# Performance work log

Measured on AMD Instinct MI355X. Metric: run time of the kernel, lower is better.

## Reference

```python
import jax, jax.numpy as jnp
import numpy as np

C = 128          # channels
N = 100000       # cells per rank (rank 0,1,2)
E_A0, E_A1, E_I1, E_I2 = 400000, 400000, 200000, 300000
NI = {"a0": 3, "a1": 6, "i1": 3, "i2": 6}   # invariant feature dims per relation
FACTOR = {"u0": 2, "u1": 3, "u2": 2}          # update-MLP concat factors


def setup_inputs() -> dict:
    key = jax.random.key(0)
    ks = iter(jax.random.split(key, 64))
    d = {}
    for name in ("f0", "f1", "f2"):
        d[name] = jax.random.normal(next(ks), (N, C), dtype=jnp.float32)
    for name, E in (("a0", E_A0), ("a1", E_A1), ("i1", E_I1), ("i2", E_I2)):
        d[name + "_send"] = jax.random.randint(next(ks), (E,), 0, N)
        d[name + "_recv"] = jax.random.randint(next(ks), (E,), 0, N)
        d["inv_" + name] = jax.random.uniform(next(ks), (E, NI[name]), dtype=jnp.float32)
        fin = 2 * C + NI[name]
        d[name + "_W1"] = jax.random.normal(next(ks), (fin, C), dtype=jnp.float32) / np.sqrt(fin)
        d[name + "_b1"] = jnp.zeros((C,), jnp.float32)
        d[name + "_W2"] = jax.random.normal(next(ks), (C, C), dtype=jnp.float32) / np.sqrt(C)
        d[name + "_b2"] = jnp.zeros((C,), jnp.float32)
        d[name + "_Wg"] = jax.random.normal(next(ks), (C, 1), dtype=jnp.float32) / np.sqrt(C)
        d[name + "_bg"] = jnp.zeros((1,), jnp.float32)
    for name, f in FACTOR.items():
        d[name + "_W1"] = jax.random.normal(next(ks), (f * C, C), dtype=jnp.float32) / np.sqrt(f * C)
        d[name + "_b1"] = jnp.zeros((C,), jnp.float32)
        d[name + "_W2"] = jax.random.normal(next(ks), (C, C), dtype=jnp.float32) / np.sqrt(C)
        d[name + "_b2"] = jnp.zeros((C,), jnp.float32)
    return d


def _econv(x_src, x_tgt, send, recv, inv, W1, b1, W2, b2, Wg, bg):
    # EConv: gather endpoints, per-edge 2-layer MLP on [x_s, x_t, invariants],
    # gated by a sigmoid edge-inference scalar (with_weighted_message=True).
    m = jnp.concatenate([x_src[send], x_tgt[recv], inv], axis=1)  # (E, 2C+ninv)
    m = jax.nn.silu(m @ W1 + b1)                                   # (E, C)
    m = jax.nn.silu(m @ W2 + b2)                                   # (E, C)
    gate = jax.nn.sigmoid(m @ Wg + bg)                             # (E, 1)
    return m * gate


def _aggregate(msg, recv, n):
    # ScatterAggregation: scatter-sum to target cells, then silu update.
    return jax.nn.silu(jax.ops.segment_sum(msg, recv, num_segments=n))


def _update(h, W1, b1, W2, b2):
    # update MLP: Linear -> SiLU -> Linear
    return jax.nn.silu(h @ W1 + b1) @ W2 + b2


def reference(f0, f1, f2,
              a0_send, a0_recv, inv_a0, a0_W1, a0_b1, a0_W2, a0_b2, a0_Wg, a0_bg,
              a1_send, a1_recv, inv_a1, a1_W1, a1_b1, a1_W2, a1_b2, a1_Wg, a1_bg,
              i1_send, i1_recv, inv_i1, i1_W1, i1_b1, i1_W2, i1_b2, i1_Wg, i1_bg,
              i2_send, i2_recv, inv_i2, i2_W1, i2_b1, i2_W2, i2_b2, i2_Wg, i2_bg,
              u0_W1, u0_b1, u0_W2, u0_b2,
              u1_W1, u1_b1, u1_W2, u1_b2,
              u2_W1, u2_b1, u2_W2, u2_b2):
    # same-rank messages (rank 0 and 1 adjacency)
    m_a0 = _aggregate(_econv(f0, f0, a0_send, a0_recv, inv_a0, a0_W1, a0_b1, a0_W2, a0_b2, a0_Wg, a0_bg), a0_recv, N)
    m_a1 = _aggregate(_econv(f1, f1, a1_send, a1_recv, inv_a1, a1_W1, a1_b1, a1_W2, a1_b2, a1_Wg, a1_bg), a1_recv, N)
    # low-to-high messages (incidence rank 0->1 and 1->2)
    m_i1 = _aggregate(_econv(f0, f1, i1_send, i1_recv, inv_i1, i1_W1, i1_b1, i1_W2, i1_b2, i1_Wg, i1_bg), i1_recv, N)
    m_i2 = _aggregate(_econv(f1, f2, i2_send, i2_recv, inv_i2, i2_W1, i2_b1, i2_W2, i2_b2, i2_Wg, i2_bg), i2_recv, N)
    # concat features with aggregated messages, update, residual add
    h0 = _update(jnp.concatenate([f0, m_a0], axis=1), u0_W1, u0_b1, u0_W2, u0_b2)
    h1 = _update(jnp.concatenate([f1, m_a1, m_i1], axis=1), u1_W1, u1_b1, u1_W2, u1_b2)
    h2 = _update(jnp.concatenate([f2, m_i2], axis=1), u2_W1, u2_b1, u2_W2, u2_b2)
    return jnp.stack([f0 + h0, f1 + h1, f2 + h2])  # (3, N, C)
```

## Files before the change

### kernel.cpp

```cpp
#include <hip/hip_runtime.h>
#include <hip/hip_bf16.h>
#include <cstdint>
#include <cstddef>

#define CDIM 128
#define NCELLS 100000
#define SCHUNK 1024

typedef __attribute__((ext_vector_type(8))) short short8;
typedef __attribute__((ext_vector_type(4))) float f32x4;

__device__ __forceinline__ unsigned short f2bf(float f) {
    unsigned u = __float_as_uint(f);
    unsigned r = u + 0x7FFFu + ((u >> 16) & 1u);
    return (unsigned short)(r >> 16);
}
__device__ __forceinline__ float bf2f(unsigned short u) {
    return __uint_as_float(((unsigned)u) << 16);
}
__device__ __forceinline__ float lo16(unsigned u) { return __uint_as_float(u << 16); }
__device__ __forceinline__ float hi16(unsigned u) { return __uint_as_float(u & 0xffff0000u); }
__device__ __forceinline__ unsigned pkbf(float lo, float hi) {
    unsigned r;
    asm("v_cvt_pk_bf16_f32 %0, %1, %2" : "=v"(r) : "v"(lo), "v"(hi));
    return r;
}
__device__ __forceinline__ unsigned short cvt1bf(float x) {
    return (unsigned short)(pkbf(x, x) & 0xffffu);
}
__device__ __forceinline__ float sigf(float x) {
    return __builtin_amdgcn_rcpf(1.f + __expf(-x));
}
__device__ __forceinline__ float siluf(float x) { return x * sigf(x); }

__device__ __forceinline__ unsigned silu2(unsigned a, unsigned b) {
    float lo = lo16(a) + lo16(b);
    float hi = hi16(a) + hi16(b);
    return pkbf(siluf(lo), siluf(hi));
}
__device__ __forceinline__ unsigned silu1(unsigned a) {
    return pkbf(siluf(lo16(a)), siluf(hi16(a)));
}

__device__ __forceinline__ void atomic_pk_bf16(void* addr, unsigned data) {
    asm volatile("global_atomic_pk_add_bf16 %0, %1, off"
                 :: "v"((unsigned long long)(uintptr_t)addr), "v"(data) : "memory");
}

__device__ __forceinline__ void load_lds16(const void* g, void* ldsbase, int lane) {
    __builtin_amdgcn_global_load_lds(
        (const __attribute__((address_space(1))) unsigned int*)(uintptr_t)g,
        (__attribute__((address_space(3))) unsigned int*)(uintptr_t)ldsbase,
        16, 0, 0);
}

struct PrepArgs {
    const float* src[14];
    int dstoff[14];
    int fin[14];
    int ktc[14];
    int tend[14];
};

__global__ void prep_kernel(PrepArgs pa, unsigned short* __restrict__ wb) {
    int tile = blockIdx.x;
    int m = 0;
    while (tile >= pa.tend[m]) m++;
    int local = tile - (m == 0 ? 0 : pa.tend[m - 1]);
    int ktc = pa.ktc[m];
    int ct = local / ktc;
    int kt = local % ktc;
    int l = threadIdx.x;
    unsigned short* dst = wb + pa.dstoff[m] + (size_t)local * 512 + l * 8;
    const float* src = pa.src[m];
    int fin = pa.fin[m];
    int col = ct * 16 + (l & 15);
#pragma unroll
    for (int i = 0; i < 8; i++) {
        int k = kt * 32 + (l >> 4) * 8 + i;
        float v = (k < fin) ? src[(size_t)k * CDIM + col] : 0.f;
        dst[i] = f2bf(v);
    }
}

__global__ void hist4_kernel(const int* __restrict__ r0, const int* __restrict__ r1,
                             const int* __restrict__ r2, const int* __restrict__ r3,
                             int E0, int E1, int E2, int E3, int* __restrict__ bins) {
    int i = blockIdx.x * blockDim.x + threadIdx.x;
    const int c1 = E0, c2 = c1 + E1, c3 = c2 + E2, c4 = c3 + E3;
    if (i >= c4) return;
    const int* r; int* b; int j;
    if (i < c1)      { r = r0; j = i;      b = bins; }
    else if (i < c2) { r = r1; j = i - c1; b = bins + (size_t)NCELLS; }
    else if (i < c3) { r = r2; j = i - c2; b = bins + (size_t)2 * NCELLS; }
    else             { r = r3; j = i - c3; b = bins + (size_t)3 * NCELLS; }
    atomicAdd(&b[r[j]], 1);
}

__global__ void scan_sum_kernel(const int* __restrict__ bins, int* __restrict__ part,
                                int NB, int nchunk) {
    const int rel = blockIdx.x / nchunk;
    const int ch  = blockIdx.x % nchunk;
    const int t = threadIdx.x;
    const int base = ch * SCHUNK;
    const int* b = bins + (size_t)rel * NB + base;
    const int lim = (NB - base < SCHUNK) ? (NB - base) : SCHUNK;
    int s = 0;
    for (int i = t; i < lim; i += 256) s += b[i];
#pragma unroll
    for (int d = 1; d < 64; d <<= 1) s += __shfl_xor(s, (unsigned)d, 64);
    __shared__ int ws[4];
    if ((t & 63) == 0) ws[t >> 6] = s;
    __syncthreads();
    if (t == 0) part[rel * nchunk + ch] = ws[0] + ws[1] + ws[2] + ws[3];
}

__global__ void scan_part_kernel(int* __restrict__ part, int* __restrict__ offs,
                                 int NB, int nchunk) {
    const int rel = blockIdx.x;
    const int t = threadIdx.x;
    const int lane = t & 63, w = t >> 6;
    int v = (t < nchunk) ? part[rel * nchunk + t] : 0;
    int x = v;
#pragma unroll
    for (int d = 1; d < 64; d <<= 1) {
        int y = __shfl_up(x, (unsigned)d, 64);
        if (lane >= d) x += y;
    }
    __shared__ int wsum[2];
    if (lane == 63) wsum[w] = x;
    __syncthreads();
    if (w == 1) x += wsum[0];
    if (t < nchunk) part[rel * nchunk + t] = x - v;
    if (t == nchunk - 1) offs[(size_t)rel * (NB + 1) + NB] = x;
}

__global__ void scan_write_kernel(const int* __restrict__ bins, const int* __restrict__ part,
                                  int* __restrict__ offs, int NB, int nchunk) {
    const int rel = blockIdx.x / nchunk;
    const int ch  = blockIdx.x % nchunk;
    const int t = threadIdx.x;
    const int lane = t & 63, w = t >> 6;
    const int base = ch * SCHUNK;
    const int* b = bins + (size_t)rel * NB + base;
    int* o = offs + (size_t)rel * (NB + 1) + base;
    const int lim = (NB - base < SCHUNK) ? (NB - base) : SCHUNK;
    const int i0 = t * 4;
    int v[4];
#pragma unroll
    for (int k = 0; k < 4; k++) v[k] = (i0 + k < lim) ? b[i0 + k] : 0;
    const int tsum = v[0] + v[1] + v[2] + v[3];
    int x = tsum;
#pragma unroll
    for (int d = 1; d < 64; d <<= 1) {
        int y = __shfl_up(x, (unsigned)d, 64);
        if (lane >= d) x += y;
    }
    __shared__ int wsum[4];
    if (lane == 63) wsum[w] = x;
    __syncthreads();
    int woff = 0;
#pragma unroll
    for (int k = 0; k < 4; k++) if (k < w) woff += wsum[k];
    int excl = woff + x - tsum + part[rel * nchunk + ch];
#pragma unroll
    for (int k = 0; k < 4; k++) {
        if (i0 + k < lim) { o[i0 + k] = excl; excl += v[k]; }
    }
}

struct RankArgs {
    const int* send[4];
    const int* recv[4];
    int*  perm[4];
    int2* pair[4];
    int E[4];
    const int* offs;
    int*       cur;
};

__global__ void rank4p_kernel(RankArgs a) {
    int i = blockIdx.x * blockDim.x + threadIdx.x;
    int rel = 0, j = i;
    while (rel < 4 && j >= a.E[rel]) { j -= a.E[rel]; rel++; }
    if (rel >= 4) return;
    int v = a.recv[rel][j];
    int p = a.offs[(size_t)rel * (NCELLS + 1) + v] +
            atomicAdd(&a.cur[(size_t)rel * NCELLS + v], 1);
    a.perm[rel][p] = j;
    a.pair[rel][p] = make_int2(a.send[rel][j], v);
}

template <bool SAME>
__global__ __launch_bounds__(256, 4)
void pgemm2_kernel(const float* __restrict__ fA, const float* __restrict__ fB,
                   const unsigned short* __restrict__ W1T, const float* __restrict__ b1,
                   unsigned short* __restrict__ PA, unsigned short* __restrict__ PB,
                   int nblk)
{
    constexpr int AS = 136;
    __shared__ unsigned short A[64 * AS];

    const bool second = !SAME && ((int)blockIdx.x >= nblk);
    const float* f = second ? fB : fA;
    const int n0 = (second ? (int)blockIdx.x - nblk : (int)blockIdx.x) * 64;

    const int t = threadIdx.x;
    {
        const int rl = t >> 2, q = t & 3;
        int n = n0 + rl; n = (n < NCELLS) ? n : (NCELLS - 1);
        const float4* sp = (const float4*)(f + (size_t)n * CDIM + q * 32);
        unsigned short* arow = A + rl * AS + q * 32;
#pragma unroll
        for (int i = 0; i < 4; i++) {
            float4 a = sp[2 * i], b = sp[2 * i + 1];
            uint4 o;
            o.x = pkbf(a.x, a.y); o.y = pkbf(a.z, a.w);
            o.z = pkbf(b.x, b.y); o.w = pkbf(b.z, b.w);
            *(uint4*)(arow + i * 8) = o;
        }
    }
    __syncthreads();

    const int l = t & 63, w = t >> 6;
    const int lr = l & 15, lg = l >> 4;
    const int wr = (w & 1) * 32, wc = (w >> 1) * 64;

    const int nhalf = SAME ? 2 : 1;
#pragma unroll
    for (int h = 0; h < nhalf; h++) {
        const bool hiHalf = SAME ? (h == 1) : second;
        const int koff = hiHalf ? 4 : 0;
        unsigned short* P = hiHalf ? PB : PA;

        f32x4 acc[2][4];
#pragma unroll
        for (int mt = 0; mt < 2; mt++)
#pragma unroll
            for (int ct = 0; ct < 4; ct++) acc[mt][ct] = (f32x4){0.f, 0.f, 0.f, 0.f};

#pragma unroll
        for (int kt = 0; kt < 4; ++kt) {
            short8 av[2];
#pragma unroll
            for (int mt = 0; mt < 2; mt++)
                av[mt] = *(const short8*)(A + (wr + mt * 16 + lr) * AS + kt * 32 + lg * 8);
#pragma unroll
            for (int ct = 0; ct < 4; ct++) {
                const int cg = (wc >> 4) + ct;
                short8 bv = *(const short8*)(W1T + ((size_t)(cg * 9 + kt + koff) * 64 + l) * 8);
                acc[0][ct] = __builtin_amdgcn_mfma_f32_16x16x32_bf16(av[0], bv, acc[0][ct], 0, 0, 0);
                acc[1][ct] = __builtin_amdgcn_mfma_f32_16x16x32_bf16(av[1], bv, acc[1][ct], 0, 0, 0);
            }
        }

        float b1c[4];
#pragma unroll
        for (int ct = 0; ct < 4; ct++) b1c[ct] = hiHalf ? b1[wc + ct * 16 + lr] : 0.f;

#pragma unroll
        for (int mt = 0; mt < 2; mt++)
#pragma unroll
            for (int j = 0; j < 4; j++) {
                const int row = wr + mt * 16 + lg * 4 + j;
                const int n2  = n0 + row;
                if (n2 < NCELLS) {
#pragma unroll
                    for (int ct = 0; ct < 4; ct++)
                        P[(size_t)n2 * CDIM + wc + ct * 16 + lr] = cvt1bf(acc[mt][ct][j] + b1c[ct]);
                }
            }
    }
}

template <int NINV>
__global__ __launch_bounds__(256, 4)
void econv_kernel(const unsigned short* __restrict__ Ps, const unsigned short* __restrict__ Pt,
                  const int* __restrict__ perm, const int2* __restrict__ pair,
                  const float* __restrict__ inv,
                  const unsigned short* __restrict__ W1T,
                  const unsigned short* __restrict__ W2T, const float* __restrict__ b2,
                  const float* __restrict__ Wg, const float* __restrict__ bg,
                  unsigned short* __restrict__ acc, int E)
{
    __shared__ unsigned short PsL[64 * 128];
    __shared__ unsigned short PtL[64 * 128];
    __shared__ unsigned short Ainv[64 * 40];
    __shared__ float gpart[64];
    __shared__ int   cellid[64];

    const int t = threadIdx.x, l = t & 63, w = t >> 6;
    const int e0 = blockIdx.x * 64;

    {
        const int slot = l & 15;
        const int rsub = l >> 4;
#pragma unroll
        for (int i = 0; i < 4; i++) {
            const int r = w * 16 + i * 4 + rsub;
            int p = e0 + r; p = (p < E) ? p : (E - 1);
            const int2 sr = pair[p];
            const int ss = slot ^ (r & 7);
            load_lds16(Ps + (size_t)sr.x * CDIM + ss * 8, PsL + (w * 16 + i * 4) * 128, l);
            load_lds16(Pt + (size_t)sr.y * CDIM + ss * 8, PtL + (w * 16 + i * 4) * 128, l);
        }
    }
    if (t < 64) {
        int p = e0 + t; p = (p < E) ? p : (E - 1);
        const int j = perm[p];
        cellid[t] = pair[p].y;
        gpart[t] = 0.f;
        unsigned short* ar = Ainv + t * 40;
        const float* ip = inv + (size_t)j * NINV;
#pragma unroll
        for (int jj = 0; jj < NINV; jj++) ar[jj] = cvt1bf(ip[jj]);
#pragma unroll
        for (int jj = NINV; jj < 32; jj++) ar[jj] = 0;
    }
    __syncthreads();

    const int lr = l & 15, lg = l >> 4;
    const int wr = (w & 1) * 32;
    const int wc = (w >> 1) * 64;

    f32x4 a1[2][4];
#pragma unroll
    for (int mt = 0; mt < 2; mt++)
#pragma unroll
        for (int ct = 0; ct < 4; ct++) a1[mt][ct] = (f32x4){0.f, 0.f, 0.f, 0.f};
    {
        short8 av[2];
#pragma unroll
        for (int mt = 0; mt < 2; mt++)
            av[mt] = *(const short8*)(Ainv + (wr + mt * 16 + lr) * 40 + lg * 8);
#pragma unroll
        for (int ct = 0; ct < 4; ct++) {
            const int cg = (wc >> 4) + ct;
            short8 bv = *(const short8*)(W1T + ((size_t)(cg * 9 + 8) * 64 + l) * 8);
            a1[0][ct] = __builtin_amdgcn_mfma_f32_16x16x32_bf16(av[0], bv, a1[0][ct], 0, 0, 0);
            a1[1][ct] = __builtin_amdgcn_mfma_f32_16x16x32_bf16(av[1], bv, a1[1][ct], 0, 0, 0);
        }
    }

#pragma unroll
    for (int ct = 0; ct < 4; ct++) {
        const int col = wc + ct * 16 + lr;
#pragma unroll
        for (int mt = 0; mt < 2; mt++)
#pragma unroll
            for (int j = 0; j < 4; j++) {
                const int row = wr + mt * 16 + lg * 4 + j;
                const int idx = row * 128 + (col ^ ((row & 7) << 3));
                PtL[idx] = cvt1bf(bf2f(PtL[idx]) + a1[mt][ct][j]);
            }
    }
    __syncthreads();

    {
        const int rl = t >> 2, q = t & 3;
        unsigned short* psrow = PsL + rl * 128;
        const unsigned short* ptrow = PtL + rl * 128;
#pragma unroll
        for (int i = 0; i < 4; i++) {
            const int sl = ((q * 4 + i) ^ (rl & 7)) * 8;
            uint4 us = *(const uint4*)(psrow + sl);
            uint4 ut = *(const uint4*)(ptrow + sl);
            uint4 o;
            o.x = silu2(us.x, ut.x);
            o.y = silu2(us.y, ut.y);
            o.z = silu2(us.z, ut.z);
            o.w = silu2(us.w, ut.w);
            *(uint4*)(psrow + sl) = o;
        }
    }
    __syncthreads();

    f32x4 a2[2][4];
#pragma unroll
    for (int mt = 0; mt < 2; mt++)
#pragma unroll
        for (int ct = 0; ct < 4; ct++) a2[mt][ct] = (f32x4){0.f, 0.f, 0.f, 0.f};

#pragma unroll
    for (int kt = 0; kt < 4; ++kt) {
        short8 av[2];
#pragma unroll
        for (int mt = 0; mt < 2; mt++) {
            const int row = wr + mt * 16 + lr;
            const int sl  = (kt * 4 + lg) ^ (row & 7);
            av[mt] = *(const short8*)(PsL + row * 128 + sl * 8);
        }
#pragma unroll
        for (int ct = 0; ct < 4; ct++) {
            const int cg = (wc >> 4) + ct;
            short8 bv = *(const short8*)(W2T + ((size_t)(cg * 4 + kt) * 64 + l) * 8);
            a2[0][ct] = __builtin_amdgcn_mfma_f32_16x16x32_bf16(av[0], bv, a2[0][ct], 0, 0, 0);
            a2[1][ct] = __builtin_amdgcn_mfma_f32_16x16x32_bf16(av[1], bv, a2[1][ct], 0, 0, 0);
        }
    }

    float wg[4], b2c[4];
#pragma unroll
    for (int ct = 0; ct < 4; ct++) {
        const int col = wc + ct * 16 + lr;
        wg[ct]  = Wg[col];
        b2c[ct] = b2[col];
    }
#pragma unroll
    for (int mt = 0; mt < 2; mt++)
#pragma unroll
        for (int ct = 0; ct < 4; ct++)
#pragma unroll
            for (int j = 0; j < 4; j++)
                a2[mt][ct][j] = siluf(a2[mt][ct][j] + b2c[ct]);

#pragma unroll
    for (int mt = 0; mt < 2; mt++)
#pragma unroll
        for (int j = 0; j < 4; j++) {
            float p = a2[mt][0][j] * wg[0] + a2[mt][1][j] * wg[1] +
                      a2[mt][2][j] * wg[2] + a2[mt][3][j] * wg[3];
            p += __shfl_xor(p, 1, 16);
            p += __shfl_xor(p, 2, 16);
            p += __shfl_xor(p, 4, 16);
            p += __shfl_xor(p, 8, 16);
            if (lr == 0) atomicAdd(&gpart[wr + mt * 16 + lg * 4 + j], p);
        }
    __syncthreads();

    const float bgs = bg[0];
#pragma unroll
    for (int mt = 0; mt < 2; mt++)
#pragma unroll
        for (int j = 0; j < 4; j++) {
            const int row = wr + mt * 16 + lg * 4 + j;
            const float g = (e0 + row < E) ? sigf(gpart[row] + bgs) : 0.f;
#pragma unroll
            for (int ct = 0; ct < 4; ct++) {
                const int col = wc + ct * 16 + lr;
                PtL[row * 128 + (col ^ ((row & 7) << 3))] = cvt1bf(a2[mt][ct][j] * g);
            }
        }
    __syncthreads();

    {
        const int base = w * 16;
        int cprev, cnext;
        if (w == 0) cprev = (e0 > 0) ? pair[e0 - 1].y : -1;
        else        cprev = cellid[base - 1];
        if (w == 3) cnext = (e0 + 64 < E) ? pair[e0 + 64].y : -1;
        else        cnext = cellid[base + 16];

        unsigned vv[16];
        int cid[16];
#pragma unroll
        for (int i = 0; i < 16; i++) {
            const int r = base + i;
            const unsigned* prow = (const unsigned*)(PtL + r * 128);
            vv[i]  = prow[l ^ ((r & 7) << 2)];
            cid[i] = cellid[r];
        }

        unsigned* acc32 = (unsigned*)acc;
        float accL = 0.f, accH = 0.f;
        bool openLeft = (cid[0] == cprev);
#pragma unroll
        for (int i = 0; i < 16; i++) {
            if (i > 0 && cid[i] != cid[i - 1]) {
                const size_t di = (size_t)cid[i - 1] * 64 + l;
                if (openLeft) atomic_pk_bf16(acc32 + di, pkbf(accL, accH));
                else          acc32[di] = pkbf(accL, accH);
                accL = 0.f; accH = 0.f; openLeft = false;
            }
            accL += lo16(vv[i]);
            accH += hi16(vv[i]);
        }
        const bool openRight = (cid[15] == cnext);
        const size_t di = (size_t)cid[15] * 64 + l;
        if (openLeft || openRight) atomic_pk_bf16(acc32 + di, pkbf(accL, accH));
        else                       acc32[di] = pkbf(accL, accH);
    }
}

template <int F>
__global__ __launch_bounds__(256, F == 3 ? 3 : 4)
void update_kernel(const float* __restrict__ f,
                   const unsigned short* __restrict__ s1, const unsigned short* __restrict__ s2,
                   const unsigned short* __restrict__ W1T, const float* __restrict__ b1,
                   const unsigned short* __restrict__ W2T, const float* __restrict__ b2,
                   float* __restrict__ out)
{
    constexpr int K   = F * CDIM;
    constexpr int KT1 = K / 32;
    constexpr int AS  = K + 8;
    constexpr int YS  = 136;
    __shared__ unsigned short U[64 * AS];
    unsigned short* Alds = U;
    unsigned short* Ylds = U;

    const int t  = threadIdx.x;
    const int n0 = blockIdx.x * 64;
    const int w = t >> 6, l = t & 63;

    {
        const int rl = t >> 2, q = t & 3;
        int n = n0 + rl; n = (n < NCELLS) ? n : (NCELLS - 1);
        unsigned short* arow = Alds + rl * AS;
        {
            const float4* sp = (const float4*)(f + (size_t)n * CDIM + q * 32);
#pragma unroll
            for (int i = 0; i < 4; i++) {
                float4 a = sp[2 * i], b = sp[2 * i + 1];
                uint4 o;
                o.x = pkbf(a.x, a.y); o.y = pkbf(a.z, a.w);
                o.z = pkbf(b.x, b.y); o.w = pkbf(b.z, b.w);
                *(uint4*)(arow + q * 32 + i * 8) = o;
            }
        }
#pragma unroll
        for (int p = 1; p < F; p++) {
            const unsigned short* accp = (p == 1) ? s1 : s2;
            const uint4* sp = (const uint4*)(accp + (size_t)n * CDIM + q * 32);
            uint4* dstv = (uint4*)(arow + p * CDIM + q * 32);
#pragma unroll
            for (int i = 0; i < 4; i++) {
                uint4 v = sp[i];
                uint4 o;
                o.x = silu1(v.x); o.y = silu1(v.y);
                o.z = silu1(v.z); o.w = silu1(v.w);
                dstv[i] = o;
            }
        }
    }
    __syncthreads();

    const int lr = l & 15, lg = l >> 4;
    const int wr = (w & 1) * 32;
    const int wc = (w >> 1) * 64;

    f32x4 a1[2][4];
#pragma unroll
    for (int mt = 0; mt < 2; mt++)
#pragma unroll
        for (int ct = 0; ct < 4; ct++) a1[mt][ct] = (f32x4){0.f, 0.f, 0.f, 0.f};

    for (int kt = 0; kt < KT1; ++kt) {
        short8 av[2];
#pragma unroll
        for (int mt = 0; mt < 2; mt++)
            av[mt] = *(const short8*)(Alds + (wr + mt * 16 + lr) * AS + kt * 32 + lg * 8);
#pragma unroll
        for (int ct = 0; ct < 4; ct++) {
            const int cg = (wc >> 4) + ct;
            short8 bv = *(const short8*)(W1T + ((size_t)(cg * KT1 + kt) * 64 + l) * 8);
            a1[0][ct] = __builtin_amdgcn_mfma_f32_16x16x32_bf16(av[0], bv, a1[0][ct], 0, 0, 0);
            a1[1][ct] = __builtin_amdgcn_mfma_f32_16x16x32_bf16(av[1], bv, a1[1][ct], 0, 0, 0);
        }
    }
    __syncthreads();

#pragma unroll
    for (int ct = 0; ct < 4; ct++) {
        const int col = wc + ct * 16 + lr;
        const float bb = b1[col];
#pragma unroll
        for (int mt = 0; mt < 2; mt++)
#pragma unroll
            for (int j = 0; j < 4; j++) {
                const int row = wr + mt * 16 + lg * 4 + j;
                Ylds[row * YS + col] = cvt1bf(siluf(a1[mt][ct][j] + bb));
            }
    }
    __syncthreads();

    f32x4 a2[2][4];
#pragma unroll
    for (int mt = 0; mt < 2; mt++)
#pragma unroll
        for (int ct = 0; ct < 4; ct++) a2[mt][ct] = (f32x4){0.f, 0.f, 0.f, 0.f};

    for (int kt = 0; kt < 4; ++kt) {
        short8 av[2];
#pragma unroll
        for (int mt = 0; mt < 2; mt++)
            av[mt] = *(const short8*)(Ylds + (wr + mt * 16 + lr) * YS + kt * 32 + lg * 8);
#pragma unroll
        for (int ct = 0; ct < 4; ct++) {
            const int cg = (wc >> 4) + ct;
            short8 bv = *(const short8*)(W2T + ((size_t)(cg * 4 + kt) * 64 + l) * 8);
            a2[0][ct] = __builtin_amdgcn_mfma_f32_16x16x32_bf16(av[0], bv, a2[0][ct], 0, 0, 0);
            a2[1][ct] = __builtin_amdgcn_mfma_f32_16x16x32_bf16(av[1], bv, a2[1][ct], 0, 0, 0);
        }
    }

    float b2c[4];
#pragma unroll
    for (int ct = 0; ct < 4; ct++) b2c[ct] = b2[wc + ct * 16 + lr];

#pragma unroll
    for (int mt = 0; mt < 2; mt++)
#pragma unroll
        for (int j = 0; j < 4; j++) {
            const int row = wr + mt * 16 + lg * 4 + j;
            const int n2  = n0 + row;
            if (n2 < NCELLS) {
#pragma unroll
                for (int ct = 0; ct < 4; ct++) {
                    const int col = wc + ct * 16 + lr;
                    out[(size_t)n2 * CDIM + col] =
                        f[(size_t)n2 * CDIM + col] + a2[mt][ct][j] + b2c[ct];
                }
            }
        }
}

extern "C" void kernel_launch(void* const* d_in, const int* in_sizes, int n_in,
                              void* d_out, int out_size, void* d_ws, size_t ws_size,
                              hipStream_t stream)
{
    const float* f0 = (const float*)d_in[0];
    const float* f1 = (const float*)d_in[1];
    const float* f2 = (const float*)d_in[2];

    const int*   a0_send = (const int*)d_in[3];
    const int*   a0_recv = (const int*)d_in[4];
    const float* inv_a0  = (const float*)d_in[5];
    const float* a0_b1   = (const float*)d_in[7];
    const float* a0_b2   = (const float*)d_in[9];
    const float* a0_Wg   = (const float*)d_in[10];
    const float* a0_bg   = (const float*)d_in[11];

    const int*   a1_send = (const int*)d_in[12];
    const int*   a1_recv = (const int*)d_in[13];
    const float* inv_a1  = (const float*)d_in[14];
    const float* a1_b1   = (const float*)d_in[16];
    const float* a1_b2   = (const float*)d_in[18];
    const float* a1_Wg   = (const float*)d_in[19];
    const float* a1_bg   = (const float*)d_in[20];

    const int*   i1_send = (const int*)d_in[21];
    const int*   i1_recv = (const int*)d_in[22];
    const float* inv_i1  = (const float*)d_in[23];
    const float* i1_b1   = (const float*)d_in[25];
    const float* i1_b2   = (const float*)d_in[27];
    const float* i1_Wg   = (const float*)d_in[28];
    const float* i1_bg   = (const float*)d_in[29];

    const int*   i2_send = (const int*)d_in[30];
    const int*   i2_recv = (const int*)d_in[31];
    const float* inv_i2  = (const float*)d_in[32];
    const float* i2_b1   = (const float*)d_in[34];
    const float* i2_b2   = (const float*)d_in[36];
    const float* i2_Wg   = (const float*)d_in[37];
    const float* i2_bg   = (const float*)d_in[38];

    const float* u0_b1 = (const float*)d_in[40];
    const float* u0_b2 = (const float*)d_in[42];
    const float* u1_b1 = (const float*)d_in[44];
    const float* u1_b2 = (const float*)d_in[46];
    const float* u2_b1 = (const float*)d_in[48];
    const float* u2_b2 = (const float*)d_in[50];

    const int E_a0 = in_sizes[3];
    const int E_a1 = in_sizes[12];
    const int E_i1 = in_sizes[21];
    const int E_i2 = in_sizes[30];
    const int Es[4] = {E_a0, E_a1, E_i1, E_i2};

    char* base = (char*)d_ws;
    size_t off = 0;
    auto alloc = [&](size_t bytes) -> char* {
        off = (off + 255) & ~(size_t)255;
        char* p = base + off;
        off += bytes;
        return p;
    };
    unsigned short* wb  = (unsigned short*)alloc(753664);
    int* offs_all = (int*)alloc((size_t)4 * (NCELLS + 1) * sizeof(int));
    int* bins_all = (int*)alloc((size_t)4 * NCELLS * sizeof(int));
    const int nchunk = (NCELLS + SCHUNK - 1) / SCHUNK;
    int* part = (int*)alloc((size_t)4 * nchunk * sizeof(int));
    int* perm[4];
    int2* pair[4];
    for (int r = 0; r < 4; r++) {
        perm[r] = (int*)alloc((size_t)Es[r] * sizeof(int));
        pair[r] = (int2*)alloc((size_t)Es[r] * sizeof(int2));
    }
    unsigned short* accA = (unsigned short*)alloc((size_t)NCELLS * CDIM * sizeof(unsigned short));
    unsigned short* accB = (unsigned short*)alloc((size_t)NCELLS * CDIM * sizeof(unsigned short));
    unsigned short* PsT = (unsigned short*)alloc((size_t)NCELLS * CDIM * sizeof(unsigned short));
    unsigned short* PtT = (unsigned short*)alloc((size_t)NCELLS * CDIM * sizeof(unsigned short));

    const int o_w1[4]  = {0, 36864, 73728, 110592};
    const int o_w2[4]  = {147456, 163840, 180224, 196608};
    const int o_uw1[3] = {212992, 245760, 294912};
    const int o_uw2[3] = {327680, 344064, 360448};

    PrepArgs pa;
    int idx = 0, cum = 0;
    auto add = [&](const void* s, int fin, int ktc, int woff) {
        pa.src[idx] = (const float*)s; pa.fin[idx] = fin; pa.ktc[idx] = ktc;
        pa.dstoff[idx] = woff; cum += ktc * 8; pa.tend[idx] = cum; idx++;
    };
    add(d_in[6],  259, 9,  o_w1[0]);
    add(d_in[15], 262, 9,  o_w1[1]);
    add(d_in[24], 259, 9,  o_w1[2]);
    add(d_in[33], 262, 9,  o_w1[3]);
    add(d_in[8],  128, 4,  o_w2[0]);
    add(d_in[17], 128, 4,  o_w2[1]);
    add(d_in[26], 128, 4,  o_w2[2]);
    add(d_in[35], 128, 4,  o_w2[3]);
    add(d_in[39], 256, 8,  o_uw1[0]);
    add(d_in[43], 384, 12, o_uw1[1]);
    add(d_in[47], 256, 8,  o_uw1[2]);
    add(d_in[41], 128, 4,  o_uw2[0]);
    add(d_in[45], 128, 4,  o_uw2[1]);
    add(d_in[49], 128, 4,  o_uw2[2]);
    prep_kernel<<<cum, 64, 0, stream>>>(pa, wb);

    const int Etot = E_a0 + E_a1 + E_i1 + E_i2;
    hipMemsetAsync(bins_all, 0, (size_t)4 * NCELLS * sizeof(int), stream);
    hist4_kernel<<<(Etot + 255) / 256, 256, 0, stream>>>(
        a0_recv, a1_recv, i1_recv, i2_recv, E_a0, E_a1, E_i1, E_i2, bins_all);
    scan_sum_kernel<<<4 * nchunk, 256, 0, stream>>>(bins_all, part, NCELLS, nchunk);
    scan_part_kernel<<<4, 128, 0, stream>>>(part, offs_all, NCELLS, nchunk);
    scan_write_kernel<<<4 * nchunk, 256, 0, stream>>>(bins_all, part, offs_all, NCELLS, nchunk);
    hipMemsetAsync(bins_all, 0, (size_t)4 * NCELLS * sizeof(int), stream);
    {
        RankArgs ra;
        const int* sends[4] = {a0_send, a1_send, i1_send, i2_send};
        const int* recvs[4] = {a0_recv, a1_recv, i1_recv, i2_recv};
        for (int r = 0; r < 4; r++) {
            ra.send[r] = sends[r]; ra.recv[r] = recvs[r];
            ra.perm[r] = perm[r]; ra.pair[r] = pair[r]; ra.E[r] = Es[r];
        }
        ra.offs = offs_all; ra.cur = bins_all;
        rank4p_kernel<<<(Etot + 255) / 256, 256, 0, stream>>>(ra);
    }

    const size_t accBytes = (size_t)NCELLS * CDIM * sizeof(unsigned short);
    hipMemsetAsync(accA, 0, accBytes, stream);
    hipMemsetAsync(accB, 0, accBytes, stream);

    float* out = (float*)d_out;
    const int UPD_BLK = (NCELLS + 63) / 64;
    const int PG_BLK  = UPD_BLK;

    pgemm2_kernel<true><<<PG_BLK, 256, 0, stream>>>(
        f0, f0, wb + o_w1[0], a0_b1, PsT, PtT, PG_BLK);
    econv_kernel<3><<<(E_a0 + 63) / 64, 256, 0, stream>>>(
        PsT, PtT, perm[0], pair[0], inv_a0,
        wb + o_w1[0], wb + o_w2[0], a0_b2, a0_Wg, a0_bg, accA, E_a0);
    update_kernel<2><<<UPD_BLK, 256, 0, stream>>>(
        f0, accA, nullptr, wb + o_uw1[0], u0_b1, wb + o_uw2[0], u0_b2, out);
    hipMemsetAsync(accA, 0, accBytes, stream);

    pgemm2_kernel<true><<<PG_BLK, 256, 0, stream>>>(
        f1, f1, wb + o_w1[1], a1_b1, PsT, PtT, PG_BLK);
    econv_kernel<6><<<(E_a1 + 63) / 64, 256, 0, stream>>>(
        PsT, PtT, perm[1], pair[1], inv_a1,
        wb + o_w1[1], wb + o_w2[1], a1_b2, a1_Wg, a1_bg, accA, E_a1);
    pgemm2_kernel<false><<<2 * PG_BLK, 256, 0, stream>>>(
        f0, f1, wb + o_w1[2], i1_b1, PsT, PtT, PG_BLK);
    econv_kernel<3><<<(E_i1 + 63) / 64, 256, 0, stream>>>(
        PsT, PtT, perm[2], pair[2], inv_i1,
        wb + o_w1[2], wb + o_w2[2], i1_b2, i1_Wg, i1_bg, accB, E_i1);
    update_kernel<3><<<UPD_BLK, 256, 0, stream>>>(
        f1, accA, accB, wb + o_uw1[1], u1_b1, wb + o_uw2[1], u1_b2,
        out + (size_t)NCELLS * CDIM);
    hipMemsetAsync(accA, 0, accBytes, stream);

    pgemm2_kernel<false><<<2 * PG_BLK, 256, 0, stream>>>(
        f1, f2, wb + o_w1[3], i2_b1, PsT, PtT, PG_BLK);
    econv_kernel<6><<<(E_i2 + 63) / 64, 256, 0, stream>>>(
        PsT, PtT, perm[3], pair[3], inv_i2,
        wb + o_w1[3], wb + o_w2[3], i2_b2, i2_Wg, i2_bg, accA, E_i2);
    update_kernel<2><<<UPD_BLK, 256, 0, stream>>>(
        f2, accA, nullptr, wb + o_uw1[2], u2_b1, wb + o_uw2[2], u2_b2,
        out + 2 * (size_t)NCELLS * CDIM);
}
```

Before: 720.9 us.

## Give each wave its own 16 edge rows to drop block-wide barriers in econv

The econv kernel's work split changes from a 2x2 grid of row and column tiles per wave to each wave owning 16 full edge rows across all 128 output columns. The per-row gate dot product can then be reduced entirely inside the wave with shuffles, which removes the shared gpart atomics and every __syncthreads, replaced by a wave-local vmcnt wait. Neighbour cell ids for segment boundaries are read from global memory instead of the shared cellid array. In exchange each wave does twice as many W1T/W2T fragment loads per MFMA and holds more accumulator registers, which may lower occupancy.

Measured after the change: 715.6 us (median of 2 runs). About the same (-0.7%).

```diff
diff --git a/kernel.cpp b/kernel.cpp
--- a/kernel.cpp
+++ b/kernel.cpp
@@ -286,78 +286,71 @@
     __shared__ unsigned short PsL[64 * 128];
     __shared__ unsigned short PtL[64 * 128];
     __shared__ unsigned short Ainv[64 * 40];
-    __shared__ float gpart[64];
-    __shared__ int   cellid[64];
+    __shared__ int cellid[64];
 
     const int t = threadIdx.x, l = t & 63, w = t >> 6;
     const int e0 = blockIdx.x * 64;
+    const int base = w * 16;
+    const int lr = l & 15, lg = l >> 4;
 
     {
         const int slot = l & 15;
         const int rsub = l >> 4;
 #pragma unroll
         for (int i = 0; i < 4; i++) {
-            const int r = w * 16 + i * 4 + rsub;
+            const int r = base + i * 4 + rsub;
             int p = e0 + r; p = (p < E) ? p : (E - 1);
             const int2 sr = pair[p];
             const int ss = slot ^ (r & 7);
-            load_lds16(Ps + (size_t)sr.x * CDIM + ss * 8, PsL + (w * 16 + i * 4) * 128, l);
-            load_lds16(Pt + (size_t)sr.y * CDIM + ss * 8, PtL + (w * 16 + i * 4) * 128, l);
-        }
-    }
-    if (t < 64) {
-        int p = e0 + t; p = (p < E) ? p : (E - 1);
-        const int j = perm[p];
-        cellid[t] = pair[p].y;
-        gpart[t] = 0.f;
-        unsigned short* ar = Ainv + t * 40;
-        const float* ip = inv + (size_t)j * NINV;
-#pragma unroll
-        for (int jj = 0; jj < NINV; jj++) ar[jj] = cvt1bf(ip[jj]);
-#pragma unroll
-        for (int jj = NINV; jj < 32; jj++) ar[jj] = 0;
-    }
-    __syncthreads();
-
-    const int lr = l & 15, lg = l >> 4;
-    const int wr = (w & 1) * 32;
-    const int wc = (w >> 1) * 64;
-
-    f32x4 a1[2][4];
-#pragma unroll
-    for (int mt = 0; mt < 2; mt++)
-#pragma unroll
-        for (int ct = 0; ct < 4; ct++) a1[mt][ct] = (f32x4){0.f, 0.f, 0.f, 0.f};
+            load_lds16(Ps + (size_t)sr.x * CDIM + ss * 8, PsL + (base + i * 4) * 128, l);
+            load_lds16(Pt + (size_t)sr.y * CDIM + ss * 8, PtL + (base + i * 4) * 128, l);
+        }
+    }
     {
-        short8 av[2];
-#pragma unroll
-        for (int mt = 0; mt < 2; mt++)
-            av[mt] = *(const short8*)(Ainv + (wr + mt * 16 + lr) * 40 + lg * 8);
-#pragma unroll
-        for (int ct = 0; ct < 4; ct++) {
-            const int cg = (wc >> 4) + ct;
+        const int r = base + lr;
+        uint4 u = make_uint4(0u, 0u, 0u, 0u);
+        if (lg == 0) {
+            int p = e0 + r; p = (p < E) ? p : (E - 1);
+            const int j = perm[p];
+            cellid[r] = pair[p].y;
+            const float* ip = inv + (size_t)j * NINV;
+            float v[8];
+#pragma unroll
+            for (int k = 0; k < 8; k++) v[k] = (k < NINV) ? ip[k] : 0.f;
+            u.x = pkbf(v[0], v[1]);
+            u.y = pkbf(v[2], v[3]);
+            u.z = pkbf(v[4], v[5]);
+            u.w = pkbf(v[6], v[7]);
+        }
+        *(uint4*)(Ainv + r * 40 + lg * 8) = u;
+    }
+    asm volatile("s_waitcnt vmcnt(0)" ::: "memory");
+
+    f32x4 a1[8];
+#pragma unroll
+    for (int cg = 0; cg < 8; cg++) a1[cg] = (f32x4){0.f, 0.f, 0.f, 0.f};
+    {
+        short8 av = *(const short8*)(Ainv + (base + lr) * 40 + lg * 8);
+#pragma unroll
+        for (int cg = 0; cg < 8; cg++) {
             short8 bv = *(const short8*)(W1T + ((size_t)(cg * 9 + 8) * 64 + l) * 8);
-            a1[0][ct] = __builtin_amdgcn_mfma_f32_16x16x32_bf16(av[0], bv, a1[0][ct], 0, 0, 0);
-            a1[1][ct] = __builtin_amdgcn_mfma_f32_16x16x32_bf16(av[1], bv, a1[1][ct], 0, 0, 0);
-        }
-    }
-
-#pragma unroll
-    for (int ct = 0; ct < 4; ct++) {
-        const int col = wc + ct * 16 + lr;
-#pragma unroll
-        for (int mt = 0; mt < 2; mt++)
-#pragma unroll
-            for (int j = 0; j < 4; j++) {
-                const int row = wr + mt * 16 + lg * 4 + j;
-                const int idx = row * 128 + (col ^ ((row & 7) << 3));
-                PtL[idx] = cvt1bf(bf2f(PtL[idx]) + a1[mt][ct][j]);
-            }
-    }
-    __syncthreads();
+            a1[cg] = __builtin_amdgcn_mfma_f32_16x16x32_bf16(av, bv, a1[cg], 0, 0, 0);
+        }
+    }
+
+#pragma unroll
+    for (int cg = 0; cg < 8; cg++) {
+        const int col = cg * 16 + lr;
+#pragma unroll
+        for (int j = 0; j < 4; j++) {
+            const int row = base + lg * 4 + j;
+            const int idx = row * 128 + (col ^ ((row & 7) << 3));
+            PtL[idx] = cvt1bf(bf2f(PtL[idx]) + a1[cg][j]);
+        }
+    }
 
     {
-        const int rl = t >> 2, q = t & 3;
+        const int rl = base + (l >> 2), q = l & 3;
         unsigned short* psrow = PsL + rl * 128;
         const unsigned short* ptrow = PtL + rl * 128;
 #pragma unroll
@@ -373,83 +366,65 @@
             *(uint4*)(psrow + sl) = o;
         }
     }
-    __syncthreads();
-
-    f32x4 a2[2][4];
-#pragma unroll
-    for (int mt = 0; mt < 2; mt++)
-#pragma unroll
-        for (int ct = 0; ct < 4; ct++) a2[mt][ct] = (f32x4){0.f, 0.f, 0.f, 0.f};
-
+
+    f32x4 a2[8];
+#pragma unroll
+    for (int cg = 0; cg < 8; cg++) a2[cg] = (f32x4){0.f, 0.f, 0.f, 0.f};
 #pragma unroll
     for (int kt = 0; kt < 4; ++kt) {
-        short8 av[2];
-#pragma unroll
-        for (int mt = 0; mt < 2; mt++) {
-            const int row = wr + mt * 16 + lr;
-            const int sl  = (kt * 4 + lg) ^ (row & 7);
-            av[mt] = *(const short8*)(PsL + row * 128 + sl * 8);
-        }
-#pragma unroll
-        for (int ct = 0; ct < 4; ct++) {
-            const int cg = (wc >> 4) + ct;
+        const int row = base + lr;
+        const int sl  = (kt * 4 + lg) ^ (row & 7);
+        short8 av = *(const short8*)(PsL + row * 128 + sl * 8);
+#pragma unroll
+        for (int cg = 0; cg < 8; cg++) {
             short8 bv = *(const short8*)(W2T + ((size_t)(cg * 4 + kt) * 64 + l) * 8);
-            a2[0][ct] = __builtin_amdgcn_mfma_f32_16x16x32_bf16(av[0], bv, a2[0][ct], 0, 0, 0);
-            a2[1][ct] = __builtin_amdgcn_mfma_f32_16x16x32_bf16(av[1], bv, a2[1][ct], 0, 0, 0);
-        }
-    }
-
-    float wg[4], b2c[4];
-#pragma unroll
-    for (int ct = 0; ct < 4; ct++) {
-        const int col = wc + ct * 16 + lr;
-        wg[ct]  = Wg[col];
-        b2c[ct] = b2[col];
-    }
-#pragma unroll
-    for (int mt = 0; mt < 2; mt++)
-#pragma unroll
-        for (int ct = 0; ct < 4; ct++)
-#pragma unroll
-            for (int j = 0; j < 4; j++)
-                a2[mt][ct][j] = siluf(a2[mt][ct][j] + b2c[ct]);
-
-#pragma unroll
-    for (int mt = 0; mt < 2; mt++)
+            a2[cg] = __builtin_amdgcn_mfma_f32_16x16x32_bf16(av, bv, a2[cg], 0, 0, 0);
+        }
+    }
+
+    float wg[8], b2c[8];
+#pragma unroll
+    for (int cg = 0; cg < 8; cg++) {
+        const int col = cg * 16 + lr;
+        wg[cg]  = Wg[col];
+        b2c[cg] = b2[col];
+    }
+#pragma unroll
+    for (int cg = 0; cg < 8; cg++)
+#pragma unroll
+        for (int j = 0; j < 4; j++)
+            a2[cg][j] = siluf(a2[cg][j] + b2c[cg]);
+
+    const float bgs = bg[0];
+    float g4[4];
+#pragma unroll
+    for (int j = 0; j < 4; j++) {
+        float p = 0.f;
+#pragma unroll
+        for (int cg = 0; cg < 8; cg++) p += a2[cg][j] * wg[cg];
+        p += __shfl_xor(p, 1, 16);
+        p += __shfl_xor(p, 2, 16);
+        p += __shfl_xor(p, 4, 16);
+        p += __shfl_xor(p, 8, 16);
+        const int row = base + lg * 4 + j;
+        g4[j] = (e0 + row < E) ? sigf(p + bgs) : 0.f;
+    }
+
+#pragma unroll
+    for (int cg = 0; cg < 8; cg++) {
+        const int col = cg * 16 + lr;
 #pragma unroll
         for (int j = 0; j < 4; j++) {
-            float p = a2[mt][0][j] * wg[0] + a2[mt][1][j] * wg[1] +
-                      a2[mt][2][j] * wg[2] + a2[mt][3][j] * wg[3];
-            p += __shfl_xor(p, 1, 16);
-            p += __shfl_xor(p, 2, 16);
-            p += __shfl_xor(p, 4, 16);
-            p += __shfl_xor(p, 8, 16);
-            if (lr == 0) atomicAdd(&gpart[wr + mt * 16 + lg * 4 + j], p);
-        }
-    __syncthreads();
-
-    const float bgs = bg[0];
-#pragma unroll
-    for (int mt = 0; mt < 2; mt++)
-#pragma unroll
-        for (int j = 0; j < 4; j++) {
-            const int row = wr + mt * 16 + lg * 4 + j;
-            const float g = (e0 + row < E) ? sigf(gpart[row] + bgs) : 0.f;
-#pragma unroll
-            for (int ct = 0; ct < 4; ct++) {
-                const int col = wc + ct * 16 + lr;
-                PtL[row * 128 + (col ^ ((row & 7) << 3))] = cvt1bf(a2[mt][ct][j] * g);
-            }
-        }
-    __syncthreads();
+            const int row = base + lg * 4 + j;
+            PtL[row * 128 + (col ^ ((row & 7) << 3))] = cvt1bf(a2[cg][j] * g4[j]);
+        }
+    }
 
     {
-        const int base = w * 16;
-        int cprev, cnext;
-        if (w == 0) cprev = (e0 > 0) ? pair[e0 - 1].y : -1;
-        else        cprev = cellid[base - 1];
-        if (w == 3) cnext = (e0 + 64 < E) ? pair[e0 + 64].y : -1;
-        else        cnext = cellid[base + 16];
+        const int pidx = e0 + base - 1;
+        const int nidx = e0 + base + 16;
+        const int cprev = (pidx >= 0) ? pair[(pidx < E) ? pidx : (E - 1)].y : -1;
+        const int cnext = (nidx < E) ? pair[nidx].y : -1;
 
         unsigned vv[16];
         int cid[16];
```
